# Optimization experiments

Hardware: AMD Instinct MI355X
Metric: run time of the kernel (lower is better)

The kernel has to match this reference:

```python
import jax, jax.numpy as jnp
import numpy as np

S = 3072        # total packed tokens
E = 1280        # d_model
H = 20          # encoder_attention_heads
D = E // H      # head_dim = 64
NSEG = 16       # number of packed audio chunks


def setup_inputs() -> dict:
    key = jax.random.key(0)
    ks = jax.random.split(key, 9)
    w = lambda k, shape: (jax.random.normal(k, shape, jnp.float32) * 0.02)
    hidden_states = jax.random.normal(ks[0], (S, E), jnp.float32)
    cu_seqlens = (jnp.arange(NSEG + 1, dtype=jnp.int32) * (S // NSEG))
    return {
        "hidden_states": hidden_states,
        "Wq": w(ks[1], (E, E)), "bq": w(ks[2], (E,)),
        "Wk": w(ks[3], (E, E)),                      # k_proj has no bias
        "Wv": w(ks[4], (E, E)), "bv": w(ks[5], (E,)),
        "Wo": w(ks[6], (E, E)), "bo": w(ks[7], (E,)),
        "cu_seqlens": cu_seqlens,
    }


def reference(hidden_states, Wq, bq, Wk, Wv, bv, Wo, bo, cu_seqlens):
    Sq, Em = hidden_states.shape
    Dh = Em // H
    # projections (torch Linear: x @ W.T + b)
    q = (hidden_states @ Wq.T + bq).reshape(Sq, H, Dh).transpose(1, 0, 2)  # [H,S,D]
    k = (hidden_states @ Wk.T).reshape(Sq, H, Dh).transpose(1, 0, 2)       # [H,S,D]
    v = (hidden_states @ Wv.T + bv).reshape(Sq, H, Dh).transpose(1, 0, 2)  # [H,S,D]
    # block-diagonal additive mask from cu_seqlens (vectorized equivalent of
    # the original Python loop): tokens attend only within their own segment.
    pos = jnp.arange(Sq)
    seg = jnp.searchsorted(cu_seqlens[1:], pos, side="right")              # segment id per token
    same = seg[:, None] == seg[None, :]                                    # [S,S]
    bias = jnp.where(same, 0.0, jnp.finfo(q.dtype).min)
    attn = jnp.einsum("hqd,hkd->hqk", q, k) / np.sqrt(Dh).astype(q.dtype)  # [H,S,S]
    attn = jax.nn.softmax(attn + bias, axis=-1)
    out = jnp.einsum("hqk,hkd->hqd", attn, v)                              # [H,S,D]
    out = out.transpose(1, 0, 2).reshape(Sq, Em)
    return out @ Wo.T + bo
```

## Files before the change

### kernel.cpp

```cpp
#include <hip/hip_runtime.h>
#include <hip/hip_bf16.h>
#include <stdint.h>

#define S_TOK 3072
#define E_DIM 1280
#define H_NUM 20
#define D_HEAD 64
#define NSEG 16

typedef __attribute__((ext_vector_type(8))) short short8;
typedef __attribute__((ext_vector_type(4))) float f32x4;

__device__ __forceinline__ unsigned short f2bf(float f){
  union { float f; unsigned int i; } u; u.f = f;
  unsigned int r = u.i + 0x7FFFu + ((u.i >> 16) & 1u);
  return (unsigned short)(r >> 16);
}

__device__ __forceinline__ void gload_lds16(const void* g, void* l){
  __builtin_amdgcn_global_load_lds((__attribute__((address_space(1))) void*)(g),
                                   (__attribute__((address_space(3))) void*)(l), 16, 0, 0);
}

__global__ void cvt_all(const float* __restrict__ hs,
                        const float* __restrict__ w0, const float* __restrict__ w1,
                        const float* __restrict__ w2, const float* __restrict__ w3,
                        unsigned short* __restrict__ hsb,
                        unsigned short* __restrict__ dqkv, unsigned short* __restrict__ dob,
                        int nHS4, int nW4){
  int i = blockIdx.x * blockDim.x + threadIdx.x;
  const float* src;
  unsigned short* dst;
  size_t sj, dj;
  if (i < nHS4){
    src = hs; dst = hsb; sj = i; dj = i;
  } else {
    int t = i - nHS4;
    int w = t / nW4;
    if (w >= 4) return;
    int j = t - w * nW4;
    src = (w == 0) ? w0 : (w == 1) ? w1 : (w == 2) ? w2 : w3;
    sj = j;
    if (w < 3){ dst = dqkv; dj = (size_t)w * nW4 + j; }
    else      { dst = dob;  dj = j; }
  }
  float4 v = reinterpret_cast<const float4*>(src)[sj];
  ushort4 o;
  o.x = f2bf(v.x); o.y = f2bf(v.y); o.z = f2bf(v.z); o.w = f2bf(v.w);
  reinterpret_cast<ushort4*>(dst)[dj] = o;
}

template<int MODE, int BLOCK>
__global__ __launch_bounds__(BLOCK, 2) void gemm_pipe(
    const unsigned short* __restrict__ A,
    const unsigned short* __restrict__ Bp,
    const float* __restrict__ bias0,
    const float* __restrict__ bias1,
    unsigned short* __restrict__ Oq,
    unsigned short* __restrict__ Ok,
    unsigned short* __restrict__ Ov,
    float* __restrict__ Of,
    int M, int N, int K)
{
  constexpr int BM = (MODE == 0) ? 256 : 128;
  constexpr int BN = BM;
  constexpr int WN = (MODE == 0) ? 4 : 2;
  constexpr int WM = (BLOCK / 64) / WN;
  constexpr int MR = BM / WM / 16;
  constexpr int NR = BN / WN / 16;
  constexpr int SLOTSZ = (BM + BN) * 32;

  __shared__ __align__(16) unsigned short SH[4 * SLOTSZ];

  const int nbn = N >> (MODE == 0 ? 8 : 7);
  const int sgn = nbn / 5;
  const int st = blockIdx.x / 20, ii = blockIdx.x % 20;
  const int bm = (st / sgn) * 4 + ii / 5;
  const int bn = (st % sgn) * 5 + ii % 5;
  const int row0 = bm * BM;
  const int col0 = bn * BN;

  const int tid  = threadIdx.x;
  const int lane = tid & 63;
  const int w    = tid >> 6;
  const int wm   = (MODE == 0) ? (w >> 2) : (w >> 1);
  const int wn   = (MODE == 0) ? (w & 3) : (w & 1);

  const f32x4 fz = {0.f, 0.f, 0.f, 0.f};
  f32x4 acc[MR][NR];
#pragma unroll
  for (int m = 0; m < MR; ++m)
#pragma unroll
    for (int n = 0; n < NR; ++n) acc[m][n] = fz;

  auto stage = [&](int slot, int t){
    unsigned short* base = SH + slot * SLOTSZ;
    const int k0 = t << 5;
#pragma unroll
    for (int i = 0; i < 4; ++i){
      int s = i * BLOCK + tid;
      int r = s >> 2, p = s & 3;
      int ks = p ^ ((r >> 1) & 3);
      const unsigned short* g = (r < BM)
          ? A  + (size_t)(row0 + r) * K + k0 + ks * 8
          : Bp + (size_t)(col0 + (r - BM)) * K + k0 + ks * 8;
      gload_lds16(g, base + s * 8);
    }
  };

  const int nk = K >> 5;
  stage(0, 0);
  stage(1, 1);
  for (int t = 0; t < nk; ++t){
    if (t == nk - 1) asm volatile("s_waitcnt vmcnt(0)" ::: "memory");
    else             asm volatile("s_waitcnt vmcnt(4)" ::: "memory");
    __builtin_amdgcn_s_barrier();
    if (t + 2 < nk) stage((t + 2) & 3, t + 2);

    const unsigned short* As = SH + (t & 3) * SLOTSZ;
    const unsigned short* Bs = As + BM * 32;
    short8 af[MR], bf[NR];
#pragma unroll
    for (int n = 0; n < NR; ++n){
      int rb = wn * (BN / WN) + n * 16 + (lane & 15);
      bf[n] = *reinterpret_cast<const short8*>(&Bs[rb * 32 + (((lane >> 4) ^ ((rb >> 1) & 3))) * 8]);
    }
#pragma unroll
    for (int m = 0; m < MR; ++m){
      int ra = wm * (BM / WM) + m * 16 + (lane & 15);
      af[m] = *reinterpret_cast<const short8*>(&As[ra * 32 + (((lane >> 4) ^ ((ra >> 1) & 3))) * 8]);
    }
    __builtin_amdgcn_s_setprio(1);
#pragma unroll
    for (int m = 0; m < MR; ++m)
#pragma unroll
      for (int n = 0; n < NR; ++n)
        acc[m][n] = __builtin_amdgcn_mfma_f32_16x16x32_bf16(af[m], bf[n], acc[m][n], 0, 0, 0);
    __builtin_amdgcn_s_setprio(0);
  }
  __syncthreads();

  if (MODE == 0){
    unsigned short* Cs = SH;
    const int CSTR = 264;
    const int mat = col0 / E_DIM;
    const int cc0 = col0 - mat * E_DIM;
    unsigned short* dst = (mat == 0) ? Oq : ((mat == 1) ? Ok : Ov);
    float bb[NR];
#pragma unroll
    for (int n = 0; n < NR; ++n){
      int cc = cc0 + wn * 64 + n * 16 + (lane & 15);
      bb[n] = (mat == 0) ? bias0[cc] : (mat == 2 ? bias1[cc] : 0.0f);
    }
#pragma unroll
    for (int ph = 0; ph < 2; ++ph){
      if (wm == ph){
#pragma unroll
        for (int m = 0; m < MR; ++m)
#pragma unroll
          for (int n = 0; n < NR; ++n)
#pragma unroll
            for (int j = 0; j < 4; ++j){
              int rr = m * 16 + (lane >> 4) * 4 + j;
              int c  = wn * 64 + n * 16 + (lane & 15);
              Cs[rr * CSTR + c] = f2bf(acc[m][n][j] + bb[n]);
            }
      }
      __syncthreads();
#pragma unroll
      for (int i = 0; i < 8; ++i){
        int tk  = i * 512 + tid;
        int p   = tk >> 10;
        int idx = tk & 1023;
        int rr  = idx >> 3, sq = idx & 7;
        short8 vv = *reinterpret_cast<const short8*>(&Cs[rr * CSTR + p * 64 + sq * 8]);
        int gr = row0 + ph * 128 + rr;
        int hh = (cc0 >> 6) + p;
        *reinterpret_cast<short8*>(&dst[((size_t)hh * S_TOK + gr) * D_HEAD + sq * 8]) = vv;
      }
      __syncthreads();
    }
  } else {
#pragma unroll
    for (int m = 0; m < MR; ++m)
#pragma unroll
      for (int n = 0; n < NR; ++n){
        int c = col0 + wn * 64 + n * 16 + (lane & 15);
        float b = bias0[c];
#pragma unroll
        for (int j = 0; j < 4; ++j){
          int r = row0 + wm * 64 + m * 16 + (lane >> 4) * 4 + j;
          Of[(size_t)r * E_DIM + c] = acc[m][n][j] + b;
        }
      }
  }
}

#define VSTR 200
#define PSTR 72
__global__ __launch_bounds__(256, 3) void attn_kernel(
    const unsigned short* __restrict__ Q,
    const unsigned short* __restrict__ Kb,
    const unsigned short* __restrict__ V,
    const int* __restrict__ cu,
    unsigned short* __restrict__ O)
{
  __shared__ __align__(16) unsigned short Vt[64*VSTR];
  __shared__ __align__(16) unsigned short Pw[4][16][PSTR];

  const int bid  = blockIdx.x;
  const int unit = bid / 3;
  const int third= bid - unit*3;
  const int h    = unit >> 4;
  const int seg  = unit & 15;
  const int s0   = cu[seg];
  const int L    = cu[seg + 1] - s0;
  if (L <= 0) return;

  const int tid  = threadIdx.x;
  const int lane = tid & 63;
  const int w    = tid >> 6;
  const int row0g = third*64 + w*16;

  const unsigned short* qh = Q  + (size_t)h * S_TOK * D_HEAD;
  const unsigned short* kh = Kb + (size_t)h * S_TOK * D_HEAD;
  const unsigned short* vh = V  + (size_t)h * S_TOK * D_HEAD;

#pragma unroll
  for (int i = 0; i < 6; ++i){
    int task = i*256 + tid;
    int sr   = task % 192;
    int grp  = task / 192;
    int svr  = s0 + (sr < L ? sr : L - 1);
    short8 vv = *reinterpret_cast<const short8*>(vh + (size_t)svr*64 + grp*8);
#pragma unroll
    for (int j = 0; j < 8; ++j) Vt[(grp*8 + j)*VSTR + sr] = (unsigned short)vv[j];
  }

  short8 qf[2];
#pragma unroll
  for (int kk = 0; kk < 2; ++kk){
    int r  = row0g + (lane & 15);
    int sr = s0 + (r < L ? r : L - 1);
    qf[kk] = *reinterpret_cast<const short8*>(qh + (size_t)sr*64 + kk*32 + (lane >> 4)*8);
  }

  __syncthreads();

  const f32x4 fz = {0.f, 0.f, 0.f, 0.f};
  const float SCL = 0.125f * 1.44269504088896f;

  f32x4 sacc[12];
#pragma unroll
  for (int nt = 0; nt < 12; ++nt) sacc[nt] = fz;

#pragma unroll
  for (int nt = 0; nt < 12; ++nt){
    int rb = nt*16 + (lane & 15);
    int sr = s0 + (rb < L ? rb : L - 1);
    const unsigned short* kr = kh + (size_t)sr*64 + (lane >> 4)*8;
    short8 kf0 = *reinterpret_cast<const short8*>(kr);
    short8 kf1 = *reinterpret_cast<const short8*>(kr + 32);
    sacc[nt] = __builtin_amdgcn_mfma_f32_16x16x32_bf16(qf[0], kf0, sacc[nt], 0, 0, 0);
    sacc[nt] = __builtin_amdgcn_mfma_f32_16x16x32_bf16(qf[1], kf1, sacc[nt], 0, 0, 0);
  }

  float rinv[4];
#pragma unroll
  for (int j = 0; j < 4; ++j){
    float mx = -1e30f;
#pragma unroll
    for (int nt = 0; nt < 12; ++nt){
      int c = nt*16 + (lane & 15);
      float vv = (c < L) ? sacc[nt][j] : -1e30f;
      sacc[nt][j] = vv;
      mx = fmaxf(mx, vv);
    }
    mx = fmaxf(mx, __shfl_xor(mx, 1, 64));
    mx = fmaxf(mx, __shfl_xor(mx, 2, 64));
    mx = fmaxf(mx, __shfl_xor(mx, 4, 64));
    mx = fmaxf(mx, __shfl_xor(mx, 8, 64));
    float sum = 0.f;
#pragma unroll
    for (int nt = 0; nt < 12; ++nt){
      float pp = exp2f((sacc[nt][j] - mx) * SCL);
      sacc[nt][j] = pp;
      sum += pp;
    }
    sum += __shfl_xor(sum, 1, 64);
    sum += __shfl_xor(sum, 2, 64);
    sum += __shfl_xor(sum, 4, 64);
    sum += __shfl_xor(sum, 8, 64);
    rinv[j] = 1.0f / sum;
  }

  f32x4 oacc[4];
#pragma unroll
  for (int nt = 0; nt < 4; ++nt) oacc[nt] = fz;

#pragma unroll
  for (int kk = 0; kk < 6; ++kk){
#pragma unroll
    for (int ntl = 0; ntl < 2; ++ntl){
      int nt = kk*2 + ntl;
#pragma unroll
      for (int j = 0; j < 4; ++j)
        Pw[w][(lane >> 4)*4 + j][ntl*16 + (lane & 15)] = f2bf(sacc[nt][j]);
    }
    short8 pf = *reinterpret_cast<const short8*>(&Pw[w][lane & 15][(lane >> 4)*8]);
#pragma unroll
    for (int nt4 = 0; nt4 < 4; ++nt4){
      int dcol = nt4*16 + (lane & 15);
      short8 vf = *reinterpret_cast<const short8*>(&Vt[dcol*VSTR + kk*32 + (lane >> 4)*8]);
      oacc[nt4] = __builtin_amdgcn_mfma_f32_16x16x32_bf16(pf, vf, oacc[nt4], 0, 0, 0);
    }
  }

#pragma unroll
  for (int nt4 = 0; nt4 < 4; ++nt4)
#pragma unroll
    for (int j = 0; j < 4; ++j)
      Pw[w][(lane >> 4)*4 + j][nt4*16 + (lane & 15)] = f2bf(oacc[nt4][j] * rinv[j]);

  {
    int r = lane >> 2;
    int gr = row0g + r;
    if (gr < L){
#pragma unroll
      for (int part = 0; part < 2; ++part){
        int c0 = (lane & 3)*16 + part*8;
        short8 vv = *reinterpret_cast<const short8*>(&Pw[w][r][c0]);
        *reinterpret_cast<short8*>(&O[(size_t)(s0 + gr) * E_DIM + h*64 + c0]) = vv;
      }
    }
  }
}

extern "C" void kernel_launch(void* const* d_in, const int* in_sizes, int n_in,
                              void* d_out, int out_size, void* d_ws, size_t ws_size,
                              hipStream_t stream)
{
  const float* hs = (const float*)d_in[0];
  const float* Wq = (const float*)d_in[1];
  const float* bq = (const float*)d_in[2];
  const float* Wk = (const float*)d_in[3];
  const float* Wv = (const float*)d_in[4];
  const float* bv = (const float*)d_in[5];
  const float* Wo = (const float*)d_in[6];
  const float* bo = (const float*)d_in[7];
  const int*   cu = (const int*)d_in[8];
  float* out = (float*)d_out;

  unsigned short* p = (unsigned short*)d_ws;
  unsigned short* hsb  = p; p += (size_t)S_TOK * E_DIM;
  unsigned short* wqkv = p; p += (size_t)3 * E_DIM * E_DIM;
  unsigned short* wob  = p; p += (size_t)E_DIM * E_DIM;
  unsigned short* qb   = p; p += (size_t)S_TOK * E_DIM;
  unsigned short* kb   = p; p += (size_t)S_TOK * E_DIM;
  unsigned short* vb   = p; p += (size_t)S_TOK * E_DIM;
  unsigned short* aob  = p; p += (size_t)S_TOK * E_DIM;

  const int nHS4 = S_TOK * E_DIM / 4;
  const int nW4  = E_DIM * E_DIM / 4;
  const int nCvt = nHS4 + 4 * nW4;
  cvt_all<<<(nCvt + 255) / 256, 256, 0, stream>>>(hs, Wq, Wk, Wv, Wo, hsb, wqkv, wob, nHS4, nW4);

  gemm_pipe<0, 512><<<(S_TOK/256) * (3*E_DIM/256), 512, 0, stream>>>(
      hsb, wqkv, bq, bv, qb, kb, vb, nullptr, S_TOK, 3*E_DIM, E_DIM);

  attn_kernel<<<H_NUM * NSEG * 3, 256, 0, stream>>>(qb, kb, vb, cu, aob);

  gemm_pipe<1, 256><<<(S_TOK/128) * (E_DIM/128), 256, 0, stream>>>(
      aob, wob, bo, nullptr, nullptr, nullptr, nullptr, out, S_TOK, E_DIM, E_DIM);
}
```

Measured before the change: 98.18 us.

## Load GEMM B operand directly from global, stage only A in LDS

Replaces the pipelined GEMM with a 128x128 tile kernel. Only the A tile goes through LDS, using a 3-slot ring with K=64 per step and an 8-way XOR swizzle. The B (weight) fragments are read straight from global memory into registers each step. Tile order changes to M-major with no grouped swizzle, and the QKV GEMM drops from 256-tile 512-thread blocks to 128-tile 256-thread blocks with occupancy 3. The aim is less LDS traffic and higher occupancy. The cost is global B loads that are not prefetched, which adds latency and relies on L2 reuse.

```diff
diff --git a/kernel.cpp b/kernel.cpp
--- a/kernel.cpp
+++ b/kernel.cpp
@@ -50,8 +50,8 @@
   reinterpret_cast<ushort4*>(dst)[dj] = o;
 }
 
-template<int MODE, int BLOCK>
-__global__ __launch_bounds__(BLOCK, 2) void gemm_pipe(
+template<int MODE>
+__global__ __launch_bounds__(256, 3) void gemm_bg(
     const unsigned short* __restrict__ A,
     const unsigned short* __restrict__ Bp,
     const float* __restrict__ bias0,
@@ -62,93 +62,82 @@
     float* __restrict__ Of,
     int M, int N, int K)
 {
-  constexpr int BM = (MODE == 0) ? 256 : 128;
-  constexpr int BN = BM;
-  constexpr int WN = (MODE == 0) ? 4 : 2;
-  constexpr int WM = (BLOCK / 64) / WN;
-  constexpr int MR = BM / WM / 16;
-  constexpr int NR = BN / WN / 16;
-  constexpr int SLOTSZ = (BM + BN) * 32;
-
-  __shared__ __align__(16) unsigned short SH[4 * SLOTSZ];
-
-  const int nbn = N >> (MODE == 0 ? 8 : 7);
-  const int sgn = nbn / 5;
-  const int st = blockIdx.x / 20, ii = blockIdx.x % 20;
-  const int bm = (st / sgn) * 4 + ii / 5;
-  const int bn = (st % sgn) * 5 + ii % 5;
-  const int row0 = bm * BM;
-  const int col0 = bn * BN;
+  __shared__ __align__(16) unsigned short SH[3 * 8192];
+
+  const int nbm = M >> 7;
+  const int bm = blockIdx.x % nbm;
+  const int bn = blockIdx.x / nbm;
+  const int row0 = bm << 7;
+  const int col0 = bn << 7;
 
   const int tid  = threadIdx.x;
   const int lane = tid & 63;
   const int w    = tid >> 6;
-  const int wm   = (MODE == 0) ? (w >> 2) : (w >> 1);
-  const int wn   = (MODE == 0) ? (w & 3) : (w & 1);
+  const int wm   = w >> 1;
+  const int wn   = w & 1;
 
   const f32x4 fz = {0.f, 0.f, 0.f, 0.f};
-  f32x4 acc[MR][NR];
-#pragma unroll
-  for (int m = 0; m < MR; ++m)
-#pragma unroll
-    for (int n = 0; n < NR; ++n) acc[m][n] = fz;
+  f32x4 acc[4][4];
+#pragma unroll
+  for (int m = 0; m < 4; ++m)
+#pragma unroll
+    for (int n = 0; n < 4; ++n) acc[m][n] = fz;
+
+  const unsigned short* Bbase = Bp + (size_t)(col0 + wn * 64 + (lane & 15)) * K + (lane >> 4) * 8;
 
   auto stage = [&](int slot, int t){
-    unsigned short* base = SH + slot * SLOTSZ;
-    const int k0 = t << 5;
+    unsigned short* dstb = SH + slot * 8192;
+    const int k0 = t << 6;
 #pragma unroll
     for (int i = 0; i < 4; ++i){
-      int s = i * BLOCK + tid;
-      int r = s >> 2, p = s & 3;
-      int ks = p ^ ((r >> 1) & 3);
-      const unsigned short* g = (r < BM)
-          ? A  + (size_t)(row0 + r) * K + k0 + ks * 8
-          : Bp + (size_t)(col0 + (r - BM)) * K + k0 + ks * 8;
-      gload_lds16(g, base + s * 8);
+      int s = i * 256 + tid;
+      int r = s >> 3, p = s & 7;
+      int ks = p ^ (r & 7);
+      gload_lds16(A + (size_t)(row0 + r) * K + k0 + ks * 8, dstb + s * 8);
     }
   };
 
-  const int nk = K >> 5;
+  const int nk = K >> 6;
   stage(0, 0);
   stage(1, 1);
   for (int t = 0; t < nk; ++t){
     if (t == nk - 1) asm volatile("s_waitcnt vmcnt(0)" ::: "memory");
     else             asm volatile("s_waitcnt vmcnt(4)" ::: "memory");
     __builtin_amdgcn_s_barrier();
-    if (t + 2 < nk) stage((t + 2) & 3, t + 2);
-
-    const unsigned short* As = SH + (t & 3) * SLOTSZ;
-    const unsigned short* Bs = As + BM * 32;
-    short8 af[MR], bf[NR];
-#pragma unroll
-    for (int n = 0; n < NR; ++n){
-      int rb = wn * (BN / WN) + n * 16 + (lane & 15);
-      bf[n] = *reinterpret_cast<const short8*>(&Bs[rb * 32 + (((lane >> 4) ^ ((rb >> 1) & 3))) * 8]);
-    }
-#pragma unroll
-    for (int m = 0; m < MR; ++m){
-      int ra = wm * (BM / WM) + m * 16 + (lane & 15);
-      af[m] = *reinterpret_cast<const short8*>(&As[ra * 32 + (((lane >> 4) ^ ((ra >> 1) & 3))) * 8]);
-    }
-    __builtin_amdgcn_s_setprio(1);
-#pragma unroll
-    for (int m = 0; m < MR; ++m)
-#pragma unroll
-      for (int n = 0; n < NR; ++n)
-        acc[m][n] = __builtin_amdgcn_mfma_f32_16x16x32_bf16(af[m], bf[n], acc[m][n], 0, 0, 0);
-    __builtin_amdgcn_s_setprio(0);
+    const unsigned short* As = SH + (t % 3) * 8192;
+#pragma unroll
+    for (int kk = 0; kk < 2; ++kk){
+      short8 bf[4], af[4];
+#pragma unroll
+      for (int n = 0; n < 4; ++n)
+        bf[n] = *reinterpret_cast<const short8*>(Bbase + (size_t)n * 16 * K + t * 64 + kk * 32);
+#pragma unroll
+      for (int m = 0; m < 4; ++m){
+        int ra = wm * 64 + m * 16 + (lane & 15);
+        int slot = kk * 4 + (lane >> 4);
+        af[m] = *reinterpret_cast<const short8*>(&As[ra * 64 + ((slot ^ (ra & 7))) * 8]);
+      }
+      __builtin_amdgcn_s_setprio(1);
+#pragma unroll
+      for (int m = 0; m < 4; ++m)
+#pragma unroll
+        for (int n = 0; n < 4; ++n)
+          acc[m][n] = __builtin_amdgcn_mfma_f32_16x16x32_bf16(af[m], bf[n], acc[m][n], 0, 0, 0);
+      __builtin_amdgcn_s_setprio(0);
+    }
+    if (t + 2 < nk) stage((t + 2) % 3, t + 2);
   }
   __syncthreads();
 
   if (MODE == 0){
     unsigned short* Cs = SH;
-    const int CSTR = 264;
+    const int CSTR = 136;
     const int mat = col0 / E_DIM;
     const int cc0 = col0 - mat * E_DIM;
     unsigned short* dst = (mat == 0) ? Oq : ((mat == 1) ? Ok : Ov);
-    float bb[NR];
-#pragma unroll
-    for (int n = 0; n < NR; ++n){
+    float bb[4];
+#pragma unroll
+    for (int n = 0; n < 4; ++n){
       int cc = cc0 + wn * 64 + n * 16 + (lane & 15);
       bb[n] = (mat == 0) ? bias0[cc] : (mat == 2 ? bias1[cc] : 0.0f);
     }
@@ -156,9 +145,9 @@
     for (int ph = 0; ph < 2; ++ph){
       if (wm == ph){
 #pragma unroll
-        for (int m = 0; m < MR; ++m)
-#pragma unroll
-          for (int n = 0; n < NR; ++n)
+        for (int m = 0; m < 4; ++m)
+#pragma unroll
+          for (int n = 0; n < 4; ++n)
 #pragma unroll
             for (int j = 0; j < 4; ++j){
               int rr = m * 16 + (lane >> 4) * 4 + j;
@@ -168,13 +157,13 @@
       }
       __syncthreads();
 #pragma unroll
-      for (int i = 0; i < 8; ++i){
-        int tk  = i * 512 + tid;
-        int p   = tk >> 10;
-        int idx = tk & 1023;
+      for (int i = 0; i < 4; ++i){
+        int tk  = i * 256 + tid;
+        int p   = tk >> 9;
+        int idx = tk & 511;
         int rr  = idx >> 3, sq = idx & 7;
         short8 vv = *reinterpret_cast<const short8*>(&Cs[rr * CSTR + p * 64 + sq * 8]);
-        int gr = row0 + ph * 128 + rr;
+        int gr = row0 + ph * 64 + rr;
         int hh = (cc0 >> 6) + p;
         *reinterpret_cast<short8*>(&dst[((size_t)hh * S_TOK + gr) * D_HEAD + sq * 8]) = vv;
       }
@@ -182,9 +171,9 @@
     }
   } else {
 #pragma unroll
-    for (int m = 0; m < MR; ++m)
-#pragma unroll
-      for (int n = 0; n < NR; ++n){
+    for (int m = 0; m < 4; ++m)
+#pragma unroll
+      for (int n = 0; n < 4; ++n){
         int c = col0 + wn * 64 + n * 16 + (lane & 15);
         float b = bias0[c];
 #pragma unroll
@@ -365,11 +354,11 @@
   const int nCvt = nHS4 + 4 * nW4;
   cvt_all<<<(nCvt + 255) / 256, 256, 0, stream>>>(hs, Wq, Wk, Wv, Wo, hsb, wqkv, wob, nHS4, nW4);
 
-  gemm_pipe<0, 512><<<(S_TOK/256) * (3*E_DIM/256), 512, 0, stream>>>(
+  gemm_bg<0><<<(S_TOK/128) * (3*E_DIM/128), 256, 0, stream>>>(
       hsb, wqkv, bq, bv, qb, kb, vb, nullptr, S_TOK, 3*E_DIM, E_DIM);
 
   attn_kernel<<<H_NUM * NSEG * 3, 256, 0, stream>>>(qb, kb, vb, cu, aob);
 
-  gemm_pipe<1, 256><<<(S_TOK/128) * (E_DIM/128), 256, 0, stream>>>(
+  gemm_bg<1><<<(S_TOK/128) * (E_DIM/128), 256, 0, stream>>>(
       aob, wob, bo, nullptr, nullptr, nullptr, nullptr, out, S_TOK, E_DIM, E_DIM);
 }
```

New measurement: 140.8 us. +43.4%, slower.

## Double-buffer GEMM register fragments to overlap LDS reads with MFMA

Applied to the files above, without the earlier changes.

The GEMM main loop is restructured into a two-step unrolled software pipeline. Fragments for the next K-tile are read from LDS into a second register set while MFMAs run on the current set, and global-to-LDS staging is issued before the wait and barrier. The aim is to hide LDS read latency behind matrix-core work. It costs extra registers, which may lower occupancy, and it assumes nk is even. The vmcnt accounting and the barrier ordering for ring-slot reuse must stay correct.

```diff
diff --git a/kernel.cpp b/kernel.cpp
--- a/kernel.cpp
+++ b/kernel.cpp
@@ -108,35 +108,60 @@
     }
   };
 
+  auto read_frags = [&](int u, short8* af, short8* bf){
+    const unsigned short* As = SH + (u & 3) * SLOTSZ;
+    const unsigned short* Bs = As + BM * 32;
+#pragma unroll
+    for (int n = 0; n < NR; ++n){
+      int rb = wn * (BN / WN) + n * 16 + (lane & 15);
+      bf[n] = *reinterpret_cast<const short8*>(&Bs[rb * 32 + (((lane >> 4) ^ ((rb >> 1) & 3))) * 8]);
+    }
+#pragma unroll
+    for (int m = 0; m < MR; ++m){
+      int ra = wm * (BM / WM) + m * 16 + (lane & 15);
+      af[m] = *reinterpret_cast<const short8*>(&As[ra * 32 + (((lane >> 4) ^ ((ra >> 1) & 3))) * 8]);
+    }
+  };
+
+  auto do_mfma = [&](const short8* af, const short8* bf){
+    __builtin_amdgcn_s_setprio(1);
+#pragma unroll
+    for (int m = 0; m < MR; ++m)
+#pragma unroll
+      for (int n = 0; n < NR; ++n)
+        acc[m][n] = __builtin_amdgcn_mfma_f32_16x16x32_bf16(af[m], bf[n], acc[m][n], 0, 0, 0);
+    __builtin_amdgcn_s_setprio(0);
+  };
+
+  short8 afA[MR], bfA[NR], afB[MR], bfB[NR];
+
   const int nk = K >> 5;
   stage(0, 0);
   stage(1, 1);
-  for (int t = 0; t < nk; ++t){
-    if (t == nk - 1) asm volatile("s_waitcnt vmcnt(0)" ::: "memory");
-    else             asm volatile("s_waitcnt vmcnt(4)" ::: "memory");
+  asm volatile("s_waitcnt vmcnt(4)" ::: "memory");
+  __builtin_amdgcn_s_barrier();
+  read_frags(0, afA, bfA);
+
+  for (int t = 0; t < nk; t += 2){
+    if (t + 2 < nk){
+      stage((t + 2) & 3, t + 2);
+      asm volatile("s_waitcnt vmcnt(4)" ::: "memory");
+    } else {
+      asm volatile("s_waitcnt vmcnt(0)" ::: "memory");
+    }
     __builtin_amdgcn_s_barrier();
-    if (t + 2 < nk) stage((t + 2) & 3, t + 2);
-
-    const unsigned short* As = SH + (t & 3) * SLOTSZ;
-    const unsigned short* Bs = As + BM * 32;
-    short8 af[MR], bf[NR];
-#pragma unroll
-    for (int n = 0; n < NR; ++n){
-      int rb = wn * (BN / WN) + n * 16 + (lane & 15);
-      bf[n] = *reinterpret_cast<const short8*>(&Bs[rb * 32 + (((lane >> 4) ^ ((rb >> 1) & 3))) * 8]);
-    }
-#pragma unroll
-    for (int m = 0; m < MR; ++m){
-      int ra = wm * (BM / WM) + m * 16 + (lane & 15);
-      af[m] = *reinterpret_cast<const short8*>(&As[ra * 32 + (((lane >> 4) ^ ((ra >> 1) & 3))) * 8]);
-    }
-    __builtin_amdgcn_s_setprio(1);
-#pragma unroll
-    for (int m = 0; m < MR; ++m)
-#pragma unroll
-      for (int n = 0; n < NR; ++n)
-        acc[m][n] = __builtin_amdgcn_mfma_f32_16x16x32_bf16(af[m], bf[n], acc[m][n], 0, 0, 0);
-    __builtin_amdgcn_s_setprio(0);
+    read_frags(t + 1, afB, bfB);
+    do_mfma(afA, bfA);
+
+    if (t + 3 < nk){
+      stage((t + 3) & 3, t + 3);
+      asm volatile("s_waitcnt vmcnt(4)" ::: "memory");
+    } else {
+      asm volatile("s_waitcnt vmcnt(0)" ::: "memory");
+    }
+    __builtin_amdgcn_s_barrier();
+    if (t + 2 < nk) read_frags(t + 2, afA, bfA);
+    do_mfma(afB, bfB);
   }
   __syncthreads();
 
```

Result: slower. 102.2 us (+4.1%).

## Use K=64 double-buffered GEMM tiles and fold Wo conversion into attention launch

Applied to the files above, without the earlier changes.

The GEMM mainloop now stages 64-wide K tiles in two LDS buffers with an 8-slot XOR swizzle, replacing the four-slot K=32 pipeline. This halves the number of barrier iterations and issues two MFMAs per fragment pair per iteration. The cost is a full vmcnt(0) wait each iteration, so the prefetch has less lead time. Separately, the Wo fp32-to-bf16 conversion moves out of the first conversion kernel into extra blocks appended to the attention launch, taking it off the critical path ahead of the QKV GEMM.

```diff
diff --git a/kernel.cpp b/kernel.cpp
--- a/kernel.cpp
+++ b/kernel.cpp
@@ -24,9 +24,9 @@
 
 __global__ void cvt_all(const float* __restrict__ hs,
                         const float* __restrict__ w0, const float* __restrict__ w1,
-                        const float* __restrict__ w2, const float* __restrict__ w3,
+                        const float* __restrict__ w2,
                         unsigned short* __restrict__ hsb,
-                        unsigned short* __restrict__ dqkv, unsigned short* __restrict__ dob,
+                        unsigned short* __restrict__ dqkv,
                         int nHS4, int nW4){
   int i = blockIdx.x * blockDim.x + threadIdx.x;
   const float* src;
@@ -37,12 +37,11 @@
   } else {
     int t = i - nHS4;
     int w = t / nW4;
-    if (w >= 4) return;
+    if (w >= 3) return;
     int j = t - w * nW4;
-    src = (w == 0) ? w0 : (w == 1) ? w1 : (w == 2) ? w2 : w3;
+    src = (w == 0) ? w0 : (w == 1) ? w1 : w2;
     sj = j;
-    if (w < 3){ dst = dqkv; dj = (size_t)w * nW4 + j; }
-    else      { dst = dob;  dj = j; }
+    dst = dqkv; dj = (size_t)w * nW4 + j;
   }
   float4 v = reinterpret_cast<const float4*>(src)[sj];
   ushort4 o;
@@ -51,7 +50,7 @@
 }
 
 template<int MODE, int BLOCK>
-__global__ __launch_bounds__(BLOCK, 2) void gemm_pipe(
+__global__ __launch_bounds__(BLOCK, 2) void gemm_k64(
     const unsigned short* __restrict__ A,
     const unsigned short* __restrict__ Bp,
     const float* __restrict__ bias0,
@@ -68,9 +67,9 @@
   constexpr int WM = (BLOCK / 64) / WN;
   constexpr int MR = BM / WM / 16;
   constexpr int NR = BN / WN / 16;
-  constexpr int SLOTSZ = (BM + BN) * 32;
-
-  __shared__ __align__(16) unsigned short SH[4 * SLOTSZ];
+  constexpr int SLOT = (BM + BN) * 64;
+
+  __shared__ __align__(16) unsigned short SH[2 * SLOT];
 
   const int nbn = N >> (MODE == 0 ? 8 : 7);
   const int sgn = nbn / 5;
@@ -93,14 +92,14 @@
 #pragma unroll
     for (int n = 0; n < NR; ++n) acc[m][n] = fz;
 
-  auto stage = [&](int slot, int t){
-    unsigned short* base = SH + slot * SLOTSZ;
-    const int k0 = t << 5;
-#pragma unroll
-    for (int i = 0; i < 4; ++i){
+  auto stage = [&](int buf, int t){
+    unsigned short* base = SH + buf * SLOT;
+    const int k0 = t << 6;
+#pragma unroll
+    for (int i = 0; i < 8; ++i){
       int s = i * BLOCK + tid;
-      int r = s >> 2, p = s & 3;
-      int ks = p ^ ((r >> 1) & 3);
+      int r = s >> 3, p = s & 7;
+      int ks = p ^ (r & 7);
       const unsigned short* g = (r < BM)
           ? A  + (size_t)(row0 + r) * K + k0 + ks * 8
           : Bp + (size_t)(col0 + (r - BM)) * K + k0 + ks * 8;
@@ -108,35 +107,45 @@
     }
   };
 
-  const int nk = K >> 5;
+  const int nk = K >> 6;
   stage(0, 0);
-  stage(1, 1);
+  int buf = 0;
   for (int t = 0; t < nk; ++t){
-    if (t == nk - 1) asm volatile("s_waitcnt vmcnt(0)" ::: "memory");
-    else             asm volatile("s_waitcnt vmcnt(4)" ::: "memory");
+    asm volatile("s_waitcnt vmcnt(0)" ::: "memory");
     __builtin_amdgcn_s_barrier();
-    if (t + 2 < nk) stage((t + 2) & 3, t + 2);
-
-    const unsigned short* As = SH + (t & 3) * SLOTSZ;
-    const unsigned short* Bs = As + BM * 32;
-    short8 af[MR], bf[NR];
+    if (t + 1 < nk) stage(buf ^ 1, t + 1);
+
+    const unsigned short* As = SH + buf * SLOT;
+    const unsigned short* Bs = As + BM * 64;
+    short8 af[MR][2], bf[NR][2];
 #pragma unroll
     for (int n = 0; n < NR; ++n){
       int rb = wn * (BN / WN) + n * 16 + (lane & 15);
-      bf[n] = *reinterpret_cast<const short8*>(&Bs[rb * 32 + (((lane >> 4) ^ ((rb >> 1) & 3))) * 8]);
+#pragma unroll
+      for (int kk = 0; kk < 2; ++kk){
+        int slot = kk * 4 + (lane >> 4);
+        bf[n][kk] = *reinterpret_cast<const short8*>(&Bs[rb * 64 + ((slot ^ (rb & 7))) * 8]);
+      }
     }
 #pragma unroll
     for (int m = 0; m < MR; ++m){
       int ra = wm * (BM / WM) + m * 16 + (lane & 15);
-      af[m] = *reinterpret_cast<const short8*>(&As[ra * 32 + (((lane >> 4) ^ ((ra >> 1) & 3))) * 8]);
+#pragma unroll
+      for (int kk = 0; kk < 2; ++kk){
+        int slot = kk * 4 + (lane >> 4);
+        af[m][kk] = *reinterpret_cast<const short8*>(&As[ra * 64 + ((slot ^ (ra & 7))) * 8]);
+      }
     }
     __builtin_amdgcn_s_setprio(1);
 #pragma unroll
-    for (int m = 0; m < MR; ++m)
-#pragma unroll
-      for (int n = 0; n < NR; ++n)
-        acc[m][n] = __builtin_amdgcn_mfma_f32_16x16x32_bf16(af[m], bf[n], acc[m][n], 0, 0, 0);
+    for (int kk = 0; kk < 2; ++kk)
+#pragma unroll
+      for (int m = 0; m < MR; ++m)
+#pragma unroll
+        for (int n = 0; n < NR; ++n)
+          acc[m][n] = __builtin_amdgcn_mfma_f32_16x16x32_bf16(af[m][kk], bf[n][kk], acc[m][n], 0, 0, 0);
     __builtin_amdgcn_s_setprio(0);
+    buf ^= 1;
   }
   __syncthreads();
 
@@ -198,17 +207,31 @@
 
 #define VSTR 200
 #define PSTR 72
+#define ATTN_BLKS (H_NUM * NSEG * 3)
 __global__ __launch_bounds__(256, 3) void attn_kernel(
     const unsigned short* __restrict__ Q,
     const unsigned short* __restrict__ Kb,
     const unsigned short* __restrict__ V,
     const int* __restrict__ cu,
-    unsigned short* __restrict__ O)
+    unsigned short* __restrict__ O,
+    const float* __restrict__ Wo,
+    unsigned short* __restrict__ wob,
+    int nW4)
 {
   __shared__ __align__(16) unsigned short Vt[64*VSTR];
   __shared__ __align__(16) unsigned short Pw[4][16][PSTR];
 
   const int bid  = blockIdx.x;
+  if (bid >= ATTN_BLKS){
+    int i = (bid - ATTN_BLKS) * 256 + threadIdx.x;
+    if (i < nW4){
+      float4 v = reinterpret_cast<const float4*>(Wo)[i];
+      ushort4 o;
+      o.x = f2bf(v.x); o.y = f2bf(v.y); o.z = f2bf(v.z); o.w = f2bf(v.w);
+      reinterpret_cast<ushort4*>(wob)[i] = o;
+    }
+    return;
+  }
   const int unit = bid / 3;
   const int third= bid - unit*3;
   const int h    = unit >> 4;
@@ -362,14 +385,16 @@
 
   const int nHS4 = S_TOK * E_DIM / 4;
   const int nW4  = E_DIM * E_DIM / 4;
-  const int nCvt = nHS4 + 4 * nW4;
-  cvt_all<<<(nCvt + 255) / 256, 256, 0, stream>>>(hs, Wq, Wk, Wv, Wo, hsb, wqkv, wob, nHS4, nW4);
-
-  gemm_pipe<0, 512><<<(S_TOK/256) * (3*E_DIM/256), 512, 0, stream>>>(
+  const int nCvt = nHS4 + 3 * nW4;
+  cvt_all<<<(nCvt + 255) / 256, 256, 0, stream>>>(hs, Wq, Wk, Wv, hsb, wqkv, nHS4, nW4);
+
+  gemm_k64<0, 512><<<(S_TOK/256) * (3*E_DIM/256), 512, 0, stream>>>(
       hsb, wqkv, bq, bv, qb, kb, vb, nullptr, S_TOK, 3*E_DIM, E_DIM);
 
-  attn_kernel<<<H_NUM * NSEG * 3, 256, 0, stream>>>(qb, kb, vb, cu, aob);
-
-  gemm_pipe<1, 256><<<(S_TOK/128) * (E_DIM/128), 256, 0, stream>>>(
+  const int cvtWoBlks = (nW4 + 255) / 256;
+  attn_kernel<<<ATTN_BLKS + cvtWoBlks, 256, 0, stream>>>(
+      qb, kb, vb, cu, aob, Wo, wob, nW4);
+
+  gemm_k64<1, 256><<<(S_TOK/128) * (E_DIM/128), 256, 0, stream>>>(
       aob, wob, bo, nullptr, nullptr, nullptr, nullptr, out, S_TOK, E_DIM, E_DIM);
 }
```

After: 97.75 us. About the same (-0.4%).
